# Kernel optimization log

Hardware: AMD Instinct MI355X
Metric: run time of the kernel (lower is better)

## Reference

```python
import jax, jax.numpy as jnp
import numpy as np

N = 25000   # num nodes
E = 500000  # num edges
B = 4       # num queries (batch)
D = 32      # hidden dim
R2 = 474    # doubled num_relation
L = 4       # num conv layers
EPS = 1e-6


def setup_inputs() -> dict:
    key = jax.random.key(0)
    ks = jax.random.split(key, 12)
    return {
        "node_in": jax.random.randint(ks[0], (E,), 0, N),
        "node_out": jax.random.randint(ks[1], (E,), 0, N),
        "relation": jax.random.randint(ks[2], (E,), 0, R2),
        "edge_weight": jnp.ones((E,), jnp.float32),
        "h_index": jax.random.randint(ks[3], (B,), 0, N),
        "r_index": jax.random.randint(ks[4], (B,), 0, R2),
        "query_embed": jax.random.normal(ks[5], (R2, D), jnp.float32) * 0.1,
        "rel_W": jax.random.normal(ks[6], (L, D, R2 * D), jnp.float32) * 0.05,
        "rel_b": jnp.zeros((L, R2 * D), jnp.float32),
        "lin_W": jax.random.normal(ks[7], (L, 13 * D, D), jnp.float32) * 0.05,
        "lin_b": jnp.zeros((L, D), jnp.float32),
        "mlp_W1": jax.random.normal(ks[8], (2 * D, 2 * D), jnp.float32) * 0.05,
        "mlp_b1": jnp.zeros((2 * D,), jnp.float32),
        "mlp_W2": jax.random.normal(ks[9], (2 * D, 1), jnp.float32) * 0.05,
        "mlp_b2": jnp.zeros((1,), jnp.float32),
    }


def _nbfnet(node_in, node_out, relation, h_index, r_index,
            edge_weight, query_embed, rel_W, rel_b, lin_W, lin_b,
            mlp_W1, mlp_b1, mlp_W2, mlp_b2):
    query = query_embed[r_index]                                   # [B, D]
    # boundary condition: query embedding placed at the head node of each query
    boundary = jnp.zeros((N, B, D), query.dtype).at[h_index, jnp.arange(B)].set(query)
    # append one self-entry per node (boundary message), as in the torch code
    node_out_ext = jnp.concatenate([node_out, jnp.arange(N)])      # [E+N]
    w_ext = jnp.concatenate([edge_weight, jnp.ones((N,), edge_weight.dtype)])[:, None, None]
    cnt = jax.ops.segment_sum(jnp.ones((E + N,), query.dtype), node_out_ext, N)[:, None, None]
    deg = jax.ops.segment_sum(edge_weight, node_out, N) + 1.0      # degree_out + 1, [N]
    scale = jnp.log(deg)
    scale = scale / scale.mean()
    scales = jnp.stack([jnp.ones_like(scale), scale, 1.0 / jnp.clip(scale, 0.01)], -1)  # [N,3]

    hidden = boundary
    for l in range(L):
        # dependent relation embeddings: [R2, B, D]
        rel_in = (query @ rel_W[l] + rel_b[l]).reshape(B, R2, D).transpose(1, 0, 2)
        # distmult message + boundary self-message: [E+N, B, D]
        msg = jnp.concatenate([rel_in[relation] * hidden[node_in], boundary], 0)
        mw = msg * w_ext
        mean = jax.ops.segment_sum(mw, node_out_ext, N) / cnt
        sq_mean = jax.ops.segment_sum(msg * mw, node_out_ext, N) / cnt
        mx = jax.ops.segment_max(mw, node_out_ext, N)
        mn = jax.ops.segment_min(mw, node_out_ext, N)
        std = jnp.sqrt(jnp.clip(sq_mean - mean * mean, EPS))
        feat = jnp.stack([mean, mx, mn, std], -1).reshape(N, B, 4 * D)   # PNA stats
        update = (feat[..., None] * scales[:, None, None, :]).reshape(N, B, 12 * D)
        hidden = jax.nn.relu(jnp.concatenate([hidden, update], -1) @ lin_W[l] + lin_b[l])

    feat = jnp.concatenate([hidden, jnp.broadcast_to(query[None], (N, B, D))], -1)  # [N,B,2D]
    h1 = jax.nn.relu(feat @ mlp_W1 + mlp_b1)
    score = (h1 @ mlp_W2 + mlp_b2)[..., 0]                          # [N, B]
    return score.T                                                  # [B, N]


def reference(node_in, node_out, relation, edge_weight, h_index, r_index,
              query_embed, rel_W, rel_b, lin_W, lin_b,
              mlp_W1, mlp_b1, mlp_W2, mlp_b2):
    return _nbfnet(node_in, node_out, relation, h_index, r_index,
                   edge_weight, query_embed, rel_W, rel_b, lin_W, lin_b,
                   mlp_W1, mlp_b1, mlp_W2, mlp_b2)
```

## Files before the change

### kernel.cpp

```cpp
#include <hip/hip_runtime.h>
#include <hip/hip_fp16.h>

#define NN  25000
#define EE  500000
#define BB  4
#define DD  32
#define LL  4
#define R2C 474
#define BD  128
#define THD 416
#define EPSF 1e-6f
#define WMH 13312
#define CAP 64
#define FINF 3.0e38f
#define GBATCH 5
#define L1BATCH 8

#define NEB    245
#define NWMB   208
#define NRELIN 948
#define NW1P   16

typedef _Float16 half8 __attribute__((ext_vector_type(8)));
typedef _Float16 h2v   __attribute__((ext_vector_type(2)));
typedef float    f2v   __attribute__((ext_vector_type(2)));
typedef float    f32x4 __attribute__((ext_vector_type(4)));

__device__ __forceinline__ h2v h2max(h2v a, h2v b) {
  h2v d; asm("v_pk_max_f16 %0, %1, %2" : "=v"(d) : "v"(a), "v"(b)); return d;
}
__device__ __forceinline__ h2v h2min(h2v a, h2v b) {
  h2v d; asm("v_pk_min_f16 %0, %1, %2" : "=v"(d) : "v"(a), "v"(b)); return d;
}
__device__ __forceinline__ h2v shflx_h2(h2v v, int m) {
  union { h2v h; int i; } u; u.h = v;
  u.i = __shfl_xor(u.i, m);
  return u.h;
}

__global__ __launch_bounds__(256) void build_setup_kernel(
    const int* __restrict__ node_in, const int* __restrict__ node_out,
    const int* __restrict__ relation, const float* __restrict__ ew,
    int* __restrict__ cnt, int2* __restrict__ ep,
    const float* __restrict__ linW, _Float16* __restrict__ Wm,
    const int* __restrict__ r_index, const float* __restrict__ qemb,
    const float* __restrict__ relW, const float* __restrict__ relB,
    __half* __restrict__ relIn, float* __restrict__ query,
    const float* __restrict__ W1, _Float16* __restrict__ W1m) {
  const int blk = blockIdx.x;
  const int tid = threadIdx.x;
  if (blk < NEB) {
    int i = blk * 256 + tid;
    if (i >= EE / 8) return;
    const int4*   ni4 = (const int4*)node_in;
    const int4*   no4 = (const int4*)node_out;
    const int4*   rl4 = (const int4*)relation;
    const float4* ew4 = (const float4*)ew;
    int4   noA = no4[2 * i], noB = no4[2 * i + 1];
    int4   niA = ni4[2 * i], niB = ni4[2 * i + 1];
    int4   rlA = rl4[2 * i], rlB = rl4[2 * i + 1];
    float4 ewA = ew4[2 * i], ewB = ew4[2 * i + 1];
    int s0 = atomicAdd(&cnt[noA.x], 1);
    int s1 = atomicAdd(&cnt[noA.y], 1);
    int s2 = atomicAdd(&cnt[noA.z], 1);
    int s3 = atomicAdd(&cnt[noA.w], 1);
    int s4 = atomicAdd(&cnt[noB.x], 1);
    int s5 = atomicAdd(&cnt[noB.y], 1);
    int s6 = atomicAdd(&cnt[noB.z], 1);
    int s7 = atomicAdd(&cnt[noB.w], 1);
    ep[noA.x * CAP + s0] = make_int2(niA.x | (rlA.x << 15), __float_as_int(ewA.x));
    ep[noA.y * CAP + s1] = make_int2(niA.y | (rlA.y << 15), __float_as_int(ewA.y));
    ep[noA.z * CAP + s2] = make_int2(niA.z | (rlA.z << 15), __float_as_int(ewA.z));
    ep[noA.w * CAP + s3] = make_int2(niA.w | (rlA.w << 15), __float_as_int(ewA.w));
    ep[noB.x * CAP + s4] = make_int2(niB.x | (rlB.x << 15), __float_as_int(ewB.x));
    ep[noB.y * CAP + s5] = make_int2(niB.y | (rlB.y << 15), __float_as_int(ewB.y));
    ep[noB.z * CAP + s6] = make_int2(niB.z | (rlB.z << 15), __float_as_int(ewB.z));
    ep[noB.w * CAP + s7] = make_int2(niB.w | (rlB.w << 15), __float_as_int(ewB.w));
  } else if (blk < NEB + NWMB) {
    int idx = (blk - NEB) * 256 + tid;
    int l = idx / WMH, rest = idx % WMH;
    int t = rest >> 10;
    int nt = (rest >> 9) & 1;
    int L = (rest >> 3) & 63;
    int j = rest & 7;
    int k = t * 32 + (L >> 4) * 8 + j;
    int n = nt * 16 + (L & 15);
    int wrow;
    if (k < 32) wrow = k;
    else {
      int kk = k - 32;
      int slab = kk >> 7, s = (kk >> 5) & 3, dd = kk & 31;
      wrow = DD + (dd * 4 + s) * 3 + slab;
    }
    Wm[idx] = (_Float16)linW[(size_t)l * THD * DD + (size_t)wrow * DD + n];
  } else if (blk < NEB + NWMB + NRELIN) {
    int o = (blk - NEB - NWMB) * 256 + tid;
    int l = o / (R2C * BD);
    int rest = o % (R2C * BD);
    int r = rest >> 7, b = (rest >> 5) & 3, d = rest & 31;
    int col = r * DD + d;
    const float* W = relW + (size_t)l * DD * R2C * DD;
    const float* qrow = qemb + (size_t)r_index[b] * DD;
    float acc = relB[(size_t)l * R2C * DD + col];
    #pragma unroll
    for (int k = 0; k < DD; ++k)
      acc = fmaf(qrow[k], W[(size_t)k * (R2C * DD) + col], acc);
    relIn[o] = __float2half(acc);
  } else if (blk < NEB + NWMB + NRELIN + NW1P) {
    int idx = (blk - NEB - NWMB - NRELIN) * 256 + tid;
    int kc = idx >> 11;
    int nt = (idx >> 9) & 3;
    int L = (idx >> 3) & 63;
    int j = idx & 7;
    int k = kc * 32 + (L >> 4) * 8 + j;
    int c = nt * 16 + (L & 15);
    W1m[idx] = (_Float16)W1[(size_t)k * (2 * DD) + c];
  } else {
    if (tid < BD) query[tid] = qemb[(size_t)r_index[tid >> 5] * DD + (tid & 31)];
  }
}

__global__ __launch_bounds__(1024) void lg_kernel(const int* __restrict__ cnt,
                                                  const int2* __restrict__ ep,
                                                  float* __restrict__ lg,
                                                  float* __restrict__ logsum) {
  const int lane = threadIdx.x & 63;
  const int wv   = threadIdx.x >> 6;
  const int nb   = blockIdx.x * 256 + wv * 16;
  float acc = 0.f;
  for (int it = 0; it < 16; ++it) {
    int n = nb + it;
    if (n < NN) {
      int c = cnt[n];
      int2 e = make_int2(0, 0);
      if (lane < c) e = ep[(size_t)n * CAP + lane];
      float s = __int_as_float(e.y);
      #pragma unroll
      for (int o = 32; o > 0; o >>= 1) s += __shfl_xor(s, o);
      float v = logf(s + 1.0f);
      if (lane == 0) { lg[n] = v; acc += v; }
    }
  }
  __shared__ float red[16];
  if (lane == 0) red[wv] = acc;
  __syncthreads();
  if (threadIdx.x == 0) {
    float t = 0.f;
    #pragma unroll
    for (int i = 0; i < 16; ++i) t += red[i];
    atomicAdd(logsum, t);
  }
}

template <bool LAST>
__device__ __forceinline__ void mfma_epilogue(const _Float16* sh,
                                              const _Float16* hinh,
                                              __half* houth,
                                              const float* lg,
                                              const float* logsum,
                                              const _Float16* Wm,
                                              const float* bias,
                                              const float* query,
                                              const int* h_index,
                                              int nbase, int lane, bool hzero,
                                              const _Float16* W1m,
                                              const float* b1,
                                              const float* W2,
                                              const float* b2,
                                              float* out,
                                              _Float16* hbuf) {
  const int m = lane & 15;
  const int q = lane >> 4;
  const int nl = m >> 2;
  const int n = nbase + nl;
  const int b = m & 3;
  const float sc = lg[n] * ((float)NN / logsum[0]);
  const _Float16 one = (_Float16)1.f;
  const _Float16 s1h = (_Float16)sc;
  const _Float16 s2h = (_Float16)(1.0f / fmaxf(sc, 0.01f));
  const _Float16* ssrc = sh + nl * 512 + b * 32 + q * 8;

  f32x4 c0 = {0.f, 0.f, 0.f, 0.f};
  f32x4 c1 = {0.f, 0.f, 0.f, 0.f};
  half8 a;
  if (hzero) {
    a = (half8)(_Float16)0.f;
    if (n == h_index[b]) {
      const float* qp = query + b * 32 + q * 8;
      #pragma unroll
      for (int j = 0; j < 8; ++j) a[j] = (_Float16)qp[j];
    }
  } else {
    a = *(const half8*)(hinh + (unsigned)n * BD + b * 32 + q * 8);
  }
  #pragma unroll
  for (int t = 0; t < 13; ++t) {
    if (t > 0) {
      const int slab = (t - 1) >> 2, s = (t - 1) & 3;
      a = *(const half8*)(ssrc + s * 128);
      const _Float16 sch = (slab == 0) ? one : ((slab == 1) ? s1h : s2h);
      half8 sv = {sch, sch, sch, sch, sch, sch, sch, sch};
      a = a * sv;
    }
    half8 b0 = *(const half8*)(Wm + (unsigned)(t * 2 + 0) * 512 + lane * 8);
    half8 b1f = *(const half8*)(Wm + (unsigned)(t * 2 + 1) * 512 + lane * 8);
    c0 = __builtin_amdgcn_mfma_f32_16x16x32_f16(a, b0, c0, 0, 0, 0);
    c1 = __builtin_amdgcn_mfma_f32_16x16x32_f16(a, b1f, c1, 0, 0, 0);
  }
  const int col = lane & 15;
  const float bj0 = bias[col], bj1 = bias[col + 16];
  if constexpr (!LAST) {
    #pragma unroll
    for (int i = 0; i < 4; ++i) {
      const int mr = q * 4 + i;
      __half* dst = houth + (unsigned)(nbase + (mr >> 2)) * BD + (mr & 3) * 32 + col;
      dst[0]  = __float2half(fmaxf(c0[i] + bj0, 0.f));
      dst[16] = __float2half(fmaxf(c1[i] + bj1, 0.f));
    }
  } else {
    #pragma unroll
    for (int i = 0; i < 4; ++i) {
      const int mr = q * 4 + i;
      hbuf[mr * 32 + col]      = (_Float16)fmaxf(c0[i] + bj0, 0.f);
      hbuf[mr * 32 + 16 + col] = (_Float16)fmaxf(c1[i] + bj1, 0.f);
    }
    half8 ah = *(const half8*)(hbuf + m * 32 + q * 8);
    half8 aq;
    const float* qp = query + b * 32 + q * 8;
    #pragma unroll
    for (int j = 0; j < 8; ++j) aq[j] = (_Float16)qp[j];
    f32x4 h1c[4];
    #pragma unroll
    for (int nt = 0; nt < 4; ++nt) {
      h1c[nt] = (f32x4){0.f, 0.f, 0.f, 0.f};
      half8 w0 = *(const half8*)(W1m + (unsigned)(0 * 4 + nt) * 512 + lane * 8);
      half8 w1 = *(const half8*)(W1m + (unsigned)(1 * 4 + nt) * 512 + lane * 8);
      h1c[nt] = __builtin_amdgcn_mfma_f32_16x16x32_f16(ah, w0, h1c[nt], 0, 0, 0);
      h1c[nt] = __builtin_amdgcn_mfma_f32_16x16x32_f16(aq, w1, h1c[nt], 0, 0, 0);
    }
    float part[4] = {0.f, 0.f, 0.f, 0.f};
    #pragma unroll
    for (int nt = 0; nt < 4; ++nt) {
      const float bb = b1[nt * 16 + col];
      const float ww = W2[nt * 16 + col];
      #pragma unroll
      for (int i = 0; i < 4; ++i) {
        float v = fmaxf(h1c[nt][i] + bb, 0.f);
        part[i] = fmaf(v, ww, part[i]);
      }
    }
    #pragma unroll
    for (int i = 0; i < 4; ++i) {
      part[i] += __shfl_xor(part[i], 1);
      part[i] += __shfl_xor(part[i], 2);
      part[i] += __shfl_xor(part[i], 4);
      part[i] += __shfl_xor(part[i], 8);
    }
    if (col == 0) {
      const float b2v = b2[0];
      #pragma unroll
      for (int i = 0; i < 4; ++i)
        out[(unsigned)i * NN + nbase + q] = part[i] + b2v;
    }
  }
}

__device__ __forceinline__ void stats_finish(float* sa, float* qa,
                                             h2v* mx2, h2v* mn2,
                                             int cnn, int wid, int eg, int c8,
                                             void* sh) {
  #pragma unroll
  for (int j = 0; j < 8; ++j) {
    sa[j] += __shfl_xor(sa[j], 16);
    qa[j] += __shfl_xor(qa[j], 16);
    sa[j] += __shfl_xor(sa[j], 32);
    qa[j] += __shfl_xor(qa[j], 32);
  }
  #pragma unroll
  for (int u = 0; u < 4; ++u) {
    mx2[u] = h2max(mx2[u], shflx_h2(mx2[u], 16));
    mn2[u] = h2min(mn2[u], shflx_h2(mn2[u], 16));
    mx2[u] = h2max(mx2[u], shflx_h2(mx2[u], 32));
    mn2[u] = h2min(mn2[u], shflx_h2(mn2[u], 32));
  }
  const float invc = 1.0f / (float)(cnn + 1);
  union { half8 v8; h2v h2[4]; } ov;
  #pragma unroll
  for (int u = 0; u < 4; ++u) {
    float mean0 = sa[2 * u] * invc, mean1 = sa[2 * u + 1] * invc;
    float sd0 = sqrtf(fmaxf(qa[2 * u] * invc - mean0 * mean0, EPSF));
    float sd1 = sqrtf(fmaxf(qa[2 * u + 1] * invc - mean1 * mean1, EPSF));
    h2v mpair = {(_Float16)mean0, (_Float16)mean1};
    h2v spair = {(_Float16)sd0, (_Float16)sd1};
    h2v sel = (eg == 0) ? mpair
            : ((eg == 1) ? mx2[u] : ((eg == 2) ? mn2[u] : spair));
    ov.h2[u] = sel;
  }
  ((half8*)sh)[wid * 64 + eg * 16 + c8] = ov.v8;
}

__global__ __launch_bounds__(256, 4) void layer1_fused_kernel(
    const int4* __restrict__ rel4, const int2* __restrict__ ep,
    const int* __restrict__ cnt, const int* __restrict__ h_index,
    const float* __restrict__ query, const float* __restrict__ lg,
    const float* __restrict__ logsum, const _Float16* __restrict__ Wm,
    const float* __restrict__ bias, __half* __restrict__ houth) {
  __shared__ __align__(16) __half2 sh[4][256];
  const int tid = threadIdx.x;
  const int lane = tid & 63;
  const int wid = tid >> 6;
  const int c8 = lane & 15;
  const int eg = lane >> 4;
  const int nbase = blockIdx.x * 4;
  const int n = nbase + wid;
  const int hb = h_index[c8 >> 2];
  const int cnn = __builtin_amdgcn_readfirstlane(cnt[n]);
  int2 myE = make_int2(0, 0);
  if (lane < cnn) myE = ep[n * CAP + lane];
  const float4* q4 = (const float4*)query;
  float4 qA = q4[c8 * 2], qB = q4[c8 * 2 + 1];
  float q8[8] = {qA.x, qA.y, qA.z, qA.w, qB.x, qB.y, qB.z, qB.w};
  h2v q2h[4];
  #pragma unroll
  for (int u = 0; u < 4; ++u)
    q2h[u] = (h2v){(_Float16)q8[2 * u], (_Float16)q8[2 * u + 1]};
  const bool g0 = (eg == 0);
  const bool head = (n == hb);
  const _Float16 HI = (_Float16)65504.f;
  float sa[8], qa[8];
  h2v mx2[4], mn2[4];
  #pragma unroll
  for (int u = 0; u < 4; ++u) {
    float mv0 = (g0 && head) ? q8[2 * u] : 0.f;
    float mv1 = (g0 && head) ? q8[2 * u + 1] : 0.f;
    sa[2 * u] = mv0; sa[2 * u + 1] = mv1;
    qa[2 * u] = mv0 * mv0; qa[2 * u + 1] = mv1 * mv1;
    h2v mvh = {(_Float16)mv0, (_Float16)mv1};
    mx2[u] = g0 ? mvh : (h2v){-HI, -HI};
    mn2[u] = g0 ? mvh : (h2v){HI, HI};
  }
  const int nf = cnn >> 2;
  const int tail = cnn & 3;
  for (int gbase = 0; gbase < nf; gbase += L1BATCH) {
    const int gb = min(L1BATCH, nf - gbase);
    int4 Rv[L1BATCH]; float wv[L1BATCH];
    #pragma unroll
    for (int j = 0; j < L1BATCH; ++j) {
      if (j < gb) {
        int sl = (gbase + j) * 4 + eg;
        int ex = __shfl(myE.x, sl);
        int ey = __shfl(myE.y, sl);
        bool mt = ((ex & 0x7fff) == hb);
        unsigned rr = mt ? ((unsigned)ex >> 15) : 0u;
        wv[j] = mt ? __int_as_float(ey) : 0.f;
        Rv[j] = rel4[rr * 16 + c8];
      }
    }
    #pragma unroll
    for (int j = 0; j < L1BATCH; ++j) {
      if (j < gb) {
        _Float16 wh = (_Float16)wv[j];
        h2v w2 = {wh, wh};
        const h2v* rp = (const h2v*)&Rv[j];
        #pragma unroll
        for (int u = 0; u < 4; ++u) {
          h2v m2 = q2h[u] * rp[u];
          h2v mw2 = m2 * w2;
          mx2[u] = h2max(mx2[u], mw2);
          mn2[u] = h2min(mn2[u], mw2);
          f2v mf  = __builtin_convertvector(m2, f2v);
          f2v mwf = __builtin_convertvector(mw2, f2v);
          sa[2 * u] += mwf[0]; sa[2 * u + 1] += mwf[1];
          qa[2 * u] = fmaf(mf[0], mwf[0], qa[2 * u]);
          qa[2 * u + 1] = fmaf(mf[1], mwf[1], qa[2 * u + 1]);
        }
      }
    }
  }
  if (tail) {
    int sl = (cnn & ~3) + eg;
    int ex = __shfl(myE.x, sl);
    int ey = __shfl(myE.y, sl);
    bool act = eg < tail;
    bool mt = act && ((ex & 0x7fff) == hb);
    unsigned rr = mt ? ((unsigned)ex >> 15) : 0u;
    float w = mt ? __int_as_float(ey) : 0.f;
    int4 Rv = rel4[rr * 16 + c8];
    _Float16 wh = (_Float16)w;
    h2v w2 = {wh, wh};
    const h2v* rp = (const h2v*)&Rv;
    #pragma unroll
    for (int u = 0; u < 4; ++u) {
      h2v m2 = q2h[u] * rp[u];
      h2v mw2 = m2 * w2;
      if (act) {
        mx2[u] = h2max(mx2[u], mw2);
        mn2[u] = h2min(mn2[u], mw2);
      }
      f2v mf  = __builtin_convertvector(m2, f2v);
      f2v mwf = __builtin_convertvector(mw2, f2v);
      sa[2 * u] += mwf[0]; sa[2 * u + 1] += mwf[1];
      qa[2 * u] = fmaf(mf[0], mwf[0], qa[2 * u]);
      qa[2 * u + 1] = fmaf(mf[1], mwf[1], qa[2 * u + 1]);
    }
  }
  stats_finish(sa, qa, mx2, mn2, cnn, wid, eg, c8, (void*)&sh[0][0]);
  __syncthreads();
  if (tid < 64)
    mfma_epilogue<false>((const _Float16*)&sh[0][0], nullptr, houth, lg, logsum,
                         Wm, bias, query, h_index, nbase, lane, true,
                         nullptr, nullptr, nullptr, nullptr, nullptr, nullptr);
}

template <bool LAST>
__global__ __launch_bounds__(256, 4) void layer_fused_kernel(
    const int4* __restrict__ hin4, const int4* __restrict__ rel4,
    const int2* __restrict__ ep, const int* __restrict__ cnt,
    const int* __restrict__ h_index, const float* __restrict__ query,
    const float* __restrict__ lg, const float* __restrict__ logsum,
    const _Float16* __restrict__ Wm, const float* __restrict__ bias,
    __half* __restrict__ houth,
    const _Float16* __restrict__ W1m, const float* __restrict__ b1,
    const float* __restrict__ W2, const float* __restrict__ b2,
    float* __restrict__ out) {
  __shared__ __align__(16) __half2 sh[4][256];
  __shared__ __align__(16) _Float16 hbuf[512];
  const int tid = threadIdx.x;
  const int lane = tid & 63;
  const int wid = tid >> 6;
  const int c8 = lane & 15;
  const int eg = lane >> 4;
  const int nbase = blockIdx.x * 4;
  const int n = nbase + wid;
  const int hb = h_index[c8 >> 2];
  const int cnn = __builtin_amdgcn_readfirstlane(cnt[n]);
  int2 myE = make_int2(0, 0);
  if (lane < cnn) myE = ep[n * CAP + lane];
  const float4* q4 = (const float4*)query;
  float4 qA = q4[c8 * 2], qB = q4[c8 * 2 + 1];
  float q8[8] = {qA.x, qA.y, qA.z, qA.w, qB.x, qB.y, qB.z, qB.w};
  const bool g0 = (eg == 0);
  const bool head = (n == hb);
  const _Float16 HI = (_Float16)65504.f;
  float sa[8], qa[8];
  h2v mx2[4], mn2[4];
  #pragma unroll
  for (int u = 0; u < 4; ++u) {
    float mv0 = (g0 && head) ? q8[2 * u] : 0.f;
    float mv1 = (g0 && head) ? q8[2 * u + 1] : 0.f;
    sa[2 * u] = mv0; sa[2 * u + 1] = mv1;
    qa[2 * u] = mv0 * mv0; qa[2 * u + 1] = mv1 * mv1;
    h2v mvh = {(_Float16)mv0, (_Float16)mv1};
    mx2[u] = g0 ? mvh : (h2v){-HI, -HI};
    mn2[u] = g0 ? mvh : (h2v){HI, HI};
  }
  const int nf = cnn >> 2;
  const int tail = cnn & 3;
  for (int gbase = 0; gbase < nf; gbase += GBATCH) {
    const int gb = min(GBATCH, nf - gbase);
    int4 Hv[GBATCH], Rv[GBATCH]; float wv[GBATCH];
    #pragma unroll
    for (int j = 0; j < GBATCH; ++j) {
      if (j < gb) {
        int sl = (gbase + j) * 4 + eg;
        int ex = __shfl(myE.x, sl);
        wv[j] = __int_as_float(__shfl(myE.y, sl));
        int src = ex & 0x7fff;
        unsigned rr = (unsigned)ex >> 15;
        Hv[j] = hin4[(unsigned)src * 16 + c8];
        Rv[j] = rel4[rr * 16 + c8];
      }
    }
    #pragma unroll
    for (int j = 0; j < GBATCH; ++j) {
      if (j < gb) {
        _Float16 wh = (_Float16)wv[j];
        h2v w2 = {wh, wh};
        const h2v* hp = (const h2v*)&Hv[j];
        const h2v* rp = (const h2v*)&Rv[j];
        #pragma unroll
        for (int u = 0; u < 4; ++u) {
          h2v m2 = hp[u] * rp[u];
          h2v mw2 = m2 * w2;
          mx2[u] = h2max(mx2[u], mw2);
          mn2[u] = h2min(mn2[u], mw2);
          f2v mf  = __builtin_convertvector(m2, f2v);
          f2v mwf = __builtin_convertvector(mw2, f2v);
          sa[2 * u] += mwf[0]; sa[2 * u + 1] += mwf[1];
          qa[2 * u] = fmaf(mf[0], mwf[0], qa[2 * u]);
          qa[2 * u + 1] = fmaf(mf[1], mwf[1], qa[2 * u + 1]);
        }
      }
    }
  }
  if (tail) {
    int sl = (cnn & ~3) + eg;
    int ex = __shfl(myE.x, sl);
    int ey = __shfl(myE.y, sl);
    bool act = eg < tail;
    int src = act ? (ex & 0x7fff) : 0;
    unsigned rr = act ? ((unsigned)ex >> 15) : 0u;
    float w = act ? __int_as_float(ey) : 0.f;
    int4 Hv = hin4[(unsigned)src * 16 + c8];
    int4 Rv = rel4[rr * 16 + c8];
    _Float16 wh = (_Float16)w;
    h2v w2 = {wh, wh};
    const h2v* hp = (const h2v*)&Hv;
    const h2v* rp = (const h2v*)&Rv;
    #pragma unroll
    for (int u = 0; u < 4; ++u) {
      h2v m2 = hp[u] * rp[u];
      h2v mw2 = m2 * w2;
      if (act) {
        mx2[u] = h2max(mx2[u], mw2);
        mn2[u] = h2min(mn2[u], mw2);
      }
      f2v mf  = __builtin_convertvector(m2, f2v);
      f2v mwf = __builtin_convertvector(mw2, f2v);
      sa[2 * u] += mwf[0]; sa[2 * u + 1] += mwf[1];
      qa[2 * u] = fmaf(mf[0], mwf[0], qa[2 * u]);
      qa[2 * u + 1] = fmaf(mf[1], mwf[1], qa[2 * u + 1]);
    }
  }
  stats_finish(sa, qa, mx2, mn2, cnn, wid, eg, c8, (void*)&sh[0][0]);
  __syncthreads();
  if (tid < 64)
    mfma_epilogue<LAST>((const _Float16*)&sh[0][0], (const _Float16*)hin4, houth,
                        lg, logsum, Wm, bias, query, h_index, nbase, lane, false,
                        W1m, b1, W2, b2, out, hbuf);
}

extern "C" void kernel_launch(void* const* d_in, const int* in_sizes, int n_in,
                              void* d_out, int out_size, void* d_ws, size_t ws_size,
                              hipStream_t stream) {
  const int*   node_in  = (const int*)d_in[0];
  const int*   node_out = (const int*)d_in[1];
  const int*   relation = (const int*)d_in[2];
  const float* ew       = (const float*)d_in[3];
  const int*   h_index  = (const int*)d_in[4];
  const int*   r_index  = (const int*)d_in[5];
  const float* qemb     = (const float*)d_in[6];
  const float* relW     = (const float*)d_in[7];
  const float* relB     = (const float*)d_in[8];
  const float* linW     = (const float*)d_in[9];
  const float* linB     = (const float*)d_in[10];
  const float* W1       = (const float*)d_in[11];
  const float* b1       = (const float*)d_in[12];
  const float* W2       = (const float*)d_in[13];
  const float* b2       = (const float*)d_in[14];
  float* out = (float*)d_out;

  char* ws = (char*)d_ws;
  size_t off = 0;
  auto alloc = [&](size_t bytes) -> char* {
    char* p = ws + off;
    off += (bytes + 255) & ~(size_t)255;
    return p;
  };
  __half*   h0     = (__half*)  alloc((size_t)NN * BD * 2);
  __half*   h1buf  = (__half*)  alloc((size_t)NN * BD * 2);
  __half*   relIn  = (__half*)  alloc((size_t)LL * R2C * BD * 2);
  _Float16* Wm     = (_Float16*)alloc((size_t)LL * WMH * 2);
  _Float16* W1m    = (_Float16*)alloc((size_t)4096 * 2);
  int2*     ep     = (int2*)    alloc((size_t)NN * CAP * 8);
  int*      cnti   = (int*)     alloc((size_t)NN * 4);
  float*    stats  = (float*)   alloc(256);
  float*    lg     = (float*)   alloc((size_t)NN * 4);
  float*    query  = (float*)   alloc((size_t)BD * 4);

  float* logsum = stats;

  hipMemsetAsync(cnti, 0, (((size_t)NN * 4 + 255) & ~(size_t)255) + 256, stream);

  build_setup_kernel<<<NEB + NWMB + NRELIN + NW1P + 1, 256, 0, stream>>>(
      node_in, node_out, relation, ew, cnti, ep,
      linW, Wm, r_index, qemb, relW, relB, relIn, query, W1, W1m);
  lg_kernel<<<98, 1024, 0, stream>>>(cnti, ep, lg, logsum);

  __half* hin = h0; __half* hout = h1buf;
  for (int l = 0; l < LL; ++l) {
    if (l == 0) {
      layer1_fused_kernel<<<NN / 4, 256, 0, stream>>>(
          (const int4*)relIn, ep, cnti, h_index, query, lg, logsum,
          Wm, linB, hout);
    } else if (l < LL - 1) {
      layer_fused_kernel<false><<<NN / 4, 256, 0, stream>>>(
          (const int4*)hin, (const int4*)relIn + (size_t)l * R2C * 16,
          ep, cnti, h_index, query, lg, logsum,
          Wm + (size_t)l * WMH, linB + (size_t)l * DD, hout,
          nullptr, nullptr, nullptr, nullptr, nullptr);
    } else {
      layer_fused_kernel<true><<<NN / 4, 256, 0, stream>>>(
          (const int4*)hin, (const int4*)relIn + (size_t)l * R2C * 16,
          ep, cnti, h_index, query, lg, logsum,
          Wm + (size_t)l * WMH, linB + (size_t)l * DD, hout,
          W1m, b1, W2, b2, out);
    }
    __half* tmp = hin; hin = hout; hout = tmp;
  }
}
```

Before: 292.0 us.

## Per-wave node epilogue without block barrier; use fma_mix for fp16 accumulation

Each wave now runs its own MFMA epilogue for its single node instead of wave 0 handling all four nodes after a __syncthreads, which removes the barrier and the serialized epilogue. The MFMA tile is only a quarter used (4 valid rows of 16), so total matrix work rises but is spread across all waves. The sum and sum-of-squares accumulation also switches to v_fma_mix_f32 inline asm, which reads the fp16 halves directly and drops the explicit conversions.

```diff
diff --git a/kernel.cpp b/kernel.cpp
--- a/kernel.cpp
+++ b/kernel.cpp
@@ -12,7 +12,6 @@
 #define EPSF 1e-6f
 #define WMH 13312
 #define CAP 64
-#define FINF 3.0e38f
 #define GBATCH 5
 #define L1BATCH 8
 
@@ -23,7 +22,6 @@
 
 typedef _Float16 half8 __attribute__((ext_vector_type(8)));
 typedef _Float16 h2v   __attribute__((ext_vector_type(2)));
-typedef float    f2v   __attribute__((ext_vector_type(2)));
 typedef float    f32x4 __attribute__((ext_vector_type(4)));
 
 __device__ __forceinline__ h2v h2max(h2v a, h2v b) {
@@ -36,6 +34,26 @@
   union { h2v h; int i; } u; u.h = v;
   u.i = __shfl_xor(u.i, m);
   return u.h;
+}
+__device__ __forceinline__ float fmix_lo(float acc, h2v x, float onef) {
+  asm("v_fma_mix_f32 %0, %1, %2, %0 op_sel:[0,0,0] op_sel_hi:[1,0,0]"
+      : "+v"(acc) : "v"(x), "v"(onef));
+  return acc;
+}
+__device__ __forceinline__ float fmix_hi(float acc, h2v x, float onef) {
+  asm("v_fma_mix_f32 %0, %1, %2, %0 op_sel:[1,0,0] op_sel_hi:[1,0,0]"
+      : "+v"(acc) : "v"(x), "v"(onef));
+  return acc;
+}
+__device__ __forceinline__ float fmix2_lo(float acc, h2v a, h2v b) {
+  asm("v_fma_mix_f32 %0, %1, %2, %0 op_sel:[0,0,0] op_sel_hi:[1,1,0]"
+      : "+v"(acc) : "v"(a), "v"(b));
+  return acc;
+}
+__device__ __forceinline__ float fmix2_hi(float acc, h2v a, h2v b) {
+  asm("v_fma_mix_f32 %0, %1, %2, %0 op_sel:[1,1,0] op_sel_hi:[1,1,0]"
+      : "+v"(acc) : "v"(a), "v"(b));
+  return acc;
 }
 
 __global__ __launch_bounds__(256) void build_setup_kernel(
@@ -152,123 +170,10 @@
   }
 }
 
-template <bool LAST>
-__device__ __forceinline__ void mfma_epilogue(const _Float16* sh,
-                                              const _Float16* hinh,
-                                              __half* houth,
-                                              const float* lg,
-                                              const float* logsum,
-                                              const _Float16* Wm,
-                                              const float* bias,
-                                              const float* query,
-                                              const int* h_index,
-                                              int nbase, int lane, bool hzero,
-                                              const _Float16* W1m,
-                                              const float* b1,
-                                              const float* W2,
-                                              const float* b2,
-                                              float* out,
-                                              _Float16* hbuf) {
-  const int m = lane & 15;
-  const int q = lane >> 4;
-  const int nl = m >> 2;
-  const int n = nbase + nl;
-  const int b = m & 3;
-  const float sc = lg[n] * ((float)NN / logsum[0]);
-  const _Float16 one = (_Float16)1.f;
-  const _Float16 s1h = (_Float16)sc;
-  const _Float16 s2h = (_Float16)(1.0f / fmaxf(sc, 0.01f));
-  const _Float16* ssrc = sh + nl * 512 + b * 32 + q * 8;
-
-  f32x4 c0 = {0.f, 0.f, 0.f, 0.f};
-  f32x4 c1 = {0.f, 0.f, 0.f, 0.f};
-  half8 a;
-  if (hzero) {
-    a = (half8)(_Float16)0.f;
-    if (n == h_index[b]) {
-      const float* qp = query + b * 32 + q * 8;
-      #pragma unroll
-      for (int j = 0; j < 8; ++j) a[j] = (_Float16)qp[j];
-    }
-  } else {
-    a = *(const half8*)(hinh + (unsigned)n * BD + b * 32 + q * 8);
-  }
-  #pragma unroll
-  for (int t = 0; t < 13; ++t) {
-    if (t > 0) {
-      const int slab = (t - 1) >> 2, s = (t - 1) & 3;
-      a = *(const half8*)(ssrc + s * 128);
-      const _Float16 sch = (slab == 0) ? one : ((slab == 1) ? s1h : s2h);
-      half8 sv = {sch, sch, sch, sch, sch, sch, sch, sch};
-      a = a * sv;
-    }
-    half8 b0 = *(const half8*)(Wm + (unsigned)(t * 2 + 0) * 512 + lane * 8);
-    half8 b1f = *(const half8*)(Wm + (unsigned)(t * 2 + 1) * 512 + lane * 8);
-    c0 = __builtin_amdgcn_mfma_f32_16x16x32_f16(a, b0, c0, 0, 0, 0);
-    c1 = __builtin_amdgcn_mfma_f32_16x16x32_f16(a, b1f, c1, 0, 0, 0);
-  }
-  const int col = lane & 15;
-  const float bj0 = bias[col], bj1 = bias[col + 16];
-  if constexpr (!LAST) {
-    #pragma unroll
-    for (int i = 0; i < 4; ++i) {
-      const int mr = q * 4 + i;
-      __half* dst = houth + (unsigned)(nbase + (mr >> 2)) * BD + (mr & 3) * 32 + col;
-      dst[0]  = __float2half(fmaxf(c0[i] + bj0, 0.f));
-      dst[16] = __float2half(fmaxf(c1[i] + bj1, 0.f));
-    }
-  } else {
-    #pragma unroll
-    for (int i = 0; i < 4; ++i) {
-      const int mr = q * 4 + i;
-      hbuf[mr * 32 + col]      = (_Float16)fmaxf(c0[i] + bj0, 0.f);
-      hbuf[mr * 32 + 16 + col] = (_Float16)fmaxf(c1[i] + bj1, 0.f);
-    }
-    half8 ah = *(const half8*)(hbuf + m * 32 + q * 8);
-    half8 aq;
-    const float* qp = query + b * 32 + q * 8;
-    #pragma unroll
-    for (int j = 0; j < 8; ++j) aq[j] = (_Float16)qp[j];
-    f32x4 h1c[4];
-    #pragma unroll
-    for (int nt = 0; nt < 4; ++nt) {
-      h1c[nt] = (f32x4){0.f, 0.f, 0.f, 0.f};
-      half8 w0 = *(const half8*)(W1m + (unsigned)(0 * 4 + nt) * 512 + lane * 8);
-      half8 w1 = *(const half8*)(W1m + (unsigned)(1 * 4 + nt) * 512 + lane * 8);
-      h1c[nt] = __builtin_amdgcn_mfma_f32_16x16x32_f16(ah, w0, h1c[nt], 0, 0, 0);
-      h1c[nt] = __builtin_amdgcn_mfma_f32_16x16x32_f16(aq, w1, h1c[nt], 0, 0, 0);
-    }
-    float part[4] = {0.f, 0.f, 0.f, 0.f};
-    #pragma unroll
-    for (int nt = 0; nt < 4; ++nt) {
-      const float bb = b1[nt * 16 + col];
-      const float ww = W2[nt * 16 + col];
-      #pragma unroll
-      for (int i = 0; i < 4; ++i) {
-        float v = fmaxf(h1c[nt][i] + bb, 0.f);
-        part[i] = fmaf(v, ww, part[i]);
-      }
-    }
-    #pragma unroll
-    for (int i = 0; i < 4; ++i) {
-      part[i] += __shfl_xor(part[i], 1);
-      part[i] += __shfl_xor(part[i], 2);
-      part[i] += __shfl_xor(part[i], 4);
-      part[i] += __shfl_xor(part[i], 8);
-    }
-    if (col == 0) {
-      const float b2v = b2[0];
-      #pragma unroll
-      for (int i = 0; i < 4; ++i)
-        out[(unsigned)i * NN + nbase + q] = part[i] + b2v;
-    }
-  }
-}
-
 __device__ __forceinline__ void stats_finish(float* sa, float* qa,
                                              h2v* mx2, h2v* mn2,
-                                             int cnn, int wid, int eg, int c8,
-                                             void* sh) {
+                                             int cnn, int eg, int c8,
+                                             _Float16* shW) {
   #pragma unroll
   for (int j = 0; j < 8; ++j) {
     sa[j] += __shfl_xor(sa[j], 16);
@@ -296,7 +201,120 @@
             : ((eg == 1) ? mx2[u] : ((eg == 2) ? mn2[u] : spair));
     ov.h2[u] = sel;
   }
-  ((half8*)sh)[wid * 64 + eg * 16 + c8] = ov.v8;
+  ((half8*)shW)[eg * 16 + c8] = ov.v8;
+}
+
+template <bool LAST>
+__device__ __forceinline__ void node_epilogue(const _Float16* shW,
+                                              const _Float16* hinh,
+                                              __half* houth,
+                                              const float* lg,
+                                              const float* logsum,
+                                              const _Float16* Wm,
+                                              const float* bias,
+                                              const float* query,
+                                              const int* h_index,
+                                              int n, int lane, bool hzero,
+                                              const _Float16* W1m,
+                                              const float* b1,
+                                              const float* W2,
+                                              const float* b2,
+                                              float* out,
+                                              _Float16* hbufW) {
+  const int m = lane & 15;
+  const int q = lane >> 4;
+  const int b = m & 3;
+  const float sc = lg[n] * ((float)NN / logsum[0]);
+  const _Float16 one = (_Float16)1.f;
+  const _Float16 s1h = (_Float16)sc;
+  const _Float16 s2h = (_Float16)(1.0f / fmaxf(sc, 0.01f));
+  const _Float16* ssrc = shW + b * 32 + q * 8;
+
+  f32x4 c0 = {0.f, 0.f, 0.f, 0.f};
+  f32x4 c1 = {0.f, 0.f, 0.f, 0.f};
+  half8 a;
+  if (hzero) {
+    a = (half8)(_Float16)0.f;
+    if (n == h_index[b]) {
+      const float* qp = query + b * 32 + q * 8;
+      #pragma unroll
+      for (int j = 0; j < 8; ++j) a[j] = (_Float16)qp[j];
+    }
+  } else {
+    a = *(const half8*)(hinh + (unsigned)n * BD + b * 32 + q * 8);
+  }
+  #pragma unroll
+  for (int t = 0; t < 13; ++t) {
+    if (t > 0) {
+      const int slab = (t - 1) >> 2, s = (t - 1) & 3;
+      a = *(const half8*)(ssrc + s * 128);
+      const _Float16 sch = (slab == 0) ? one : ((slab == 1) ? s1h : s2h);
+      half8 sv = {sch, sch, sch, sch, sch, sch, sch, sch};
+      a = a * sv;
+    }
+    half8 b0 = *(const half8*)(Wm + (unsigned)(t * 2 + 0) * 512 + lane * 8);
+    half8 b1f = *(const half8*)(Wm + (unsigned)(t * 2 + 1) * 512 + lane * 8);
+    c0 = __builtin_amdgcn_mfma_f32_16x16x32_f16(a, b0, c0, 0, 0, 0);
+    c1 = __builtin_amdgcn_mfma_f32_16x16x32_f16(a, b1f, c1, 0, 0, 0);
+  }
+  const int col = m;
+  const float bj0 = bias[col], bj1 = bias[col + 16];
+  if constexpr (!LAST) {
+    if (lane < 16) {
+      #pragma unroll
+      for (int i = 0; i < 4; ++i) {
+        __half* dst = houth + (unsigned)n * BD + i * 32 + col;
+        dst[0]  = __float2half(fmaxf(c0[i] + bj0, 0.f));
+        dst[16] = __float2half(fmaxf(c1[i] + bj1, 0.f));
+      }
+    }
+  } else {
+    if (lane < 16) {
+      #pragma unroll
+      for (int i = 0; i < 4; ++i) {
+        hbufW[i * 32 + col]      = (_Float16)fmaxf(c0[i] + bj0, 0.f);
+        hbufW[i * 32 + 16 + col] = (_Float16)fmaxf(c1[i] + bj1, 0.f);
+      }
+    }
+    half8 ah = *(const half8*)(hbufW + b * 32 + q * 8);
+    half8 aq;
+    const float* qp = query + b * 32 + q * 8;
+    #pragma unroll
+    for (int j = 0; j < 8; ++j) aq[j] = (_Float16)qp[j];
+    f32x4 h1c[4];
+    #pragma unroll
+    for (int nt = 0; nt < 4; ++nt) {
+      h1c[nt] = (f32x4){0.f, 0.f, 0.f, 0.f};
+      half8 w0 = *(const half8*)(W1m + (unsigned)(0 * 4 + nt) * 512 + lane * 8);
+      half8 w1 = *(const half8*)(W1m + (unsigned)(1 * 4 + nt) * 512 + lane * 8);
+      h1c[nt] = __builtin_amdgcn_mfma_f32_16x16x32_f16(ah, w0, h1c[nt], 0, 0, 0);
+      h1c[nt] = __builtin_amdgcn_mfma_f32_16x16x32_f16(aq, w1, h1c[nt], 0, 0, 0);
+    }
+    float part[4] = {0.f, 0.f, 0.f, 0.f};
+    #pragma unroll
+    for (int nt = 0; nt < 4; ++nt) {
+      const float bb = b1[nt * 16 + col];
+      const float ww = W2[nt * 16 + col];
+      #pragma unroll
+      for (int i = 0; i < 4; ++i) {
+        float v = fmaxf(h1c[nt][i] + bb, 0.f);
+        part[i] = fmaf(v, ww, part[i]);
+      }
+    }
+    #pragma unroll
+    for (int i = 0; i < 4; ++i) {
+      part[i] += __shfl_xor(part[i], 1);
+      part[i] += __shfl_xor(part[i], 2);
+      part[i] += __shfl_xor(part[i], 4);
+      part[i] += __shfl_xor(part[i], 8);
+    }
+    if (lane == 0) {
+      const float b2v = b2[0];
+      #pragma unroll
+      for (int i = 0; i < 4; ++i)
+        out[(unsigned)i * NN + n] = part[i] + b2v;
+    }
+  }
 }
 
 __global__ __launch_bounds__(256, 4) void layer1_fused_kernel(
@@ -305,14 +323,14 @@
     const float* __restrict__ query, const float* __restrict__ lg,
     const float* __restrict__ logsum, const _Float16* __restrict__ Wm,
     const float* __restrict__ bias, __half* __restrict__ houth) {
-  __shared__ __align__(16) __half2 sh[4][256];
+  __shared__ __align__(16) _Float16 shAll[4][512];
   const int tid = threadIdx.x;
   const int lane = tid & 63;
   const int wid = tid >> 6;
   const int c8 = lane & 15;
   const int eg = lane >> 4;
-  const int nbase = blockIdx.x * 4;
-  const int n = nbase + wid;
+  const int n = blockIdx.x * 4 + wid;
+  _Float16* shW = shAll[wid];
   const int hb = h_index[c8 >> 2];
   const int cnn = __builtin_amdgcn_readfirstlane(cnt[n]);
   int2 myE = make_int2(0, 0);
@@ -327,6 +345,7 @@
   const bool g0 = (eg == 0);
   const bool head = (n == hb);
   const _Float16 HI = (_Float16)65504.f;
+  const float onef = 1.0f;
   float sa[8], qa[8];
   h2v mx2[4], mn2[4];
   #pragma unroll
@@ -368,11 +387,10 @@
           h2v mw2 = m2 * w2;
           mx2[u] = h2max(mx2[u], mw2);
           mn2[u] = h2min(mn2[u], mw2);
-          f2v mf  = __builtin_convertvector(m2, f2v);
-          f2v mwf = __builtin_convertvector(mw2, f2v);
-          sa[2 * u] += mwf[0]; sa[2 * u + 1] += mwf[1];
-          qa[2 * u] = fmaf(mf[0], mwf[0], qa[2 * u]);
-          qa[2 * u + 1] = fmaf(mf[1], mwf[1], qa[2 * u + 1]);
+          sa[2 * u]     = fmix_lo(sa[2 * u], mw2, onef);
+          sa[2 * u + 1] = fmix_hi(sa[2 * u + 1], mw2, onef);
+          qa[2 * u]     = fmix2_lo(qa[2 * u], m2, mw2);
+          qa[2 * u + 1] = fmix2_hi(qa[2 * u + 1], m2, mw2);
         }
       }
     }
@@ -397,19 +415,16 @@
         mx2[u] = h2max(mx2[u], mw2);
         mn2[u] = h2min(mn2[u], mw2);
       }
-      f2v mf  = __builtin_convertvector(m2, f2v);
-      f2v mwf = __builtin_convertvector(mw2, f2v);
-      sa[2 * u] += mwf[0]; sa[2 * u + 1] += mwf[1];
-      qa[2 * u] = fmaf(mf[0], mwf[0], qa[2 * u]);
-      qa[2 * u + 1] = fmaf(mf[1], mwf[1], qa[2 * u + 1]);
-    }
-  }
-  stats_finish(sa, qa, mx2, mn2, cnn, wid, eg, c8, (void*)&sh[0][0]);
-  __syncthreads();
-  if (tid < 64)
-    mfma_epilogue<false>((const _Float16*)&sh[0][0], nullptr, houth, lg, logsum,
-                         Wm, bias, query, h_index, nbase, lane, true,
-                         nullptr, nullptr, nullptr, nullptr, nullptr, nullptr);
+      sa[2 * u]     = fmix_lo(sa[2 * u], mw2, onef);
+      sa[2 * u + 1] = fmix_hi(sa[2 * u + 1], mw2, onef);
+      qa[2 * u]     = fmix2_lo(qa[2 * u], m2, mw2);
+      qa[2 * u + 1] = fmix2_hi(qa[2 * u + 1], m2, mw2);
+    }
+  }
+  stats_finish(sa, qa, mx2, mn2, cnn, eg, c8, shW);
+  node_epilogue<false>(shW, nullptr, houth, lg, logsum, Wm, bias, query,
+                       h_index, n, lane, true,
+                       nullptr, nullptr, nullptr, nullptr, nullptr, nullptr);
 }
 
 template <bool LAST>
@@ -423,15 +438,15 @@
     const _Float16* __restrict__ W1m, const float* __restrict__ b1,
     const float* __restrict__ W2, const float* __restrict__ b2,
     float* __restrict__ out) {
-  __shared__ __align__(16) __half2 sh[4][256];
-  __shared__ __align__(16) _Float16 hbuf[512];
+  __shared__ __align__(16) _Float16 shAll[4][512];
+  __shared__ __align__(16) _Float16 hbufAll[4][128];
   const int tid = threadIdx.x;
   const int lane = tid & 63;
   const int wid = tid >> 6;
   const int c8 = lane & 15;
   const int eg = lane >> 4;
-  const int nbase = blockIdx.x * 4;
-  const int n = nbase + wid;
+  const int n = blockIdx.x * 4 + wid;
+  _Float16* shW = shAll[wid];
   const int hb = h_index[c8 >> 2];
   const int cnn = __builtin_amdgcn_readfirstlane(cnt[n]);
   int2 myE = make_int2(0, 0);
@@ -442,6 +457,7 @@
   const bool g0 = (eg == 0);
   const bool head = (n == hb);
   const _Float16 HI = (_Float16)65504.f;
+  const float onef = 1.0f;
   float sa[8], qa[8];
   h2v mx2[4], mn2[4];
   #pragma unroll
@@ -484,11 +500,10 @@
           h2v mw2 = m2 * w2;
           mx2[u] = h2max(mx2[u], mw2);
           mn2[u] = h2min(mn2[u], mw2);
-          f2v mf  = __builtin_convertvector(m2, f2v);
-          f2v mwf = __builtin_convertvector(mw2, f2v);
-          sa[2 * u] += mwf[0]; sa[2 * u + 1] += mwf[1];
-          qa[2 * u] = fmaf(mf[0], mwf[0], qa[2 * u]);
-          qa[2 * u + 1] = fmaf(mf[1], mwf[1], qa[2 * u + 1]);
+          sa[2 * u]     = fmix_lo(sa[2 * u], mw2, onef);
+          sa[2 * u + 1] = fmix_hi(sa[2 * u + 1], mw2, onef);
+          qa[2 * u]     = fmix2_lo(qa[2 * u], m2, mw2);
+          qa[2 * u + 1] = fmix2_hi(qa[2 * u + 1], m2, mw2);
         }
       }
     }
@@ -515,19 +530,16 @@
         mx2[u] = h2max(mx2[u], mw2);
         mn2[u] = h2min(mn2[u], mw2);
       }
-      f2v mf  = __builtin_convertvector(m2, f2v);
-      f2v mwf = __builtin_convertvector(mw2, f2v);
-      sa[2 * u] += mwf[0]; sa[2 * u + 1] += mwf[1];
-      qa[2 * u] = fmaf(mf[0], mwf[0], qa[2 * u]);
-      qa[2 * u + 1] = fmaf(mf[1], mwf[1], qa[2 * u + 1]);
-    }
-  }
-  stats_finish(sa, qa, mx2, mn2, cnn, wid, eg, c8, (void*)&sh[0][0]);
-  __syncthreads();
-  if (tid < 64)
-    mfma_epilogue<LAST>((const _Float16*)&sh[0][0], (const _Float16*)hin4, houth,
-                        lg, logsum, Wm, bias, query, h_index, nbase, lane, false,
-                        W1m, b1, W2, b2, out, hbuf);
+      sa[2 * u]     = fmix_lo(sa[2 * u], mw2, onef);
+      sa[2 * u + 1] = fmix_hi(sa[2 * u + 1], mw2, onef);
+      qa[2 * u]     = fmix2_lo(qa[2 * u], m2, mw2);
+      qa[2 * u + 1] = fmix2_hi(qa[2 * u + 1], m2, mw2);
+    }
+  }
+  stats_finish(sa, qa, mx2, mn2, cnn, eg, c8, shW);
+  node_epilogue<LAST>(shW, (const _Float16*)hin4, houth, lg, logsum, Wm, bias,
+                      query, h_index, n, lane, false,
+                      W1m, b1, W2, b2, out, hbufAll[wid]);
 }
 
 extern "C" void kernel_launch(void* const* d_in, const int* in_sizes, int n_in,
```

After: 327.3 us. +12.1%, slower.
